# Performance work log

Hardware: AMD Instinct MI355X
Metric: run time of the kernel (lower is better)

## Reference

```python
import jax, jax.numpy as jnp
import numpy as np

N, F, H, F_ = 8192, 256, 2, 64
NEG_MASK = -1e10
LEAKY_SLOPE = 0.2


def setup_inputs() -> dict:
    key = jax.random.key(0)
    k0, k1, k2, k3 = jax.random.split(key, 4)
    X = jax.random.normal(k0, (N, F), jnp.float32)
    A = (jax.random.uniform(k1, (N, N)) < 0.01).astype(jnp.float32)
    A = jnp.maximum(A, jnp.eye(N, dtype=jnp.float32))
    W = jax.random.normal(k2, (H, F, F_), jnp.float32) * (1.0 / np.sqrt(F))
    b = jnp.zeros((H, F_), jnp.float32)
    a = jax.random.normal(k3, (H, F_), jnp.float32) * 0.1
    return {"X": X, "A": A, "W": W, "b": b, "a": a}


def reference(X, A, W, b, a):
    # per-head projected features: [H, N, F_]
    feats = jnp.einsum('nf,hfo->hno', X, W)
    # score[h,i,j] = sum_o feats[h,i,o] * feats[h,j,o] * a[h,o]
    # (identical math to Dot(axes=-1)([X_0*X_1, a^T]) without the [N,N,F_] tensor)
    scores = jnp.einsum('hno,hmo->hnm', feats * a[:, None, :], feats)
    scores = jax.nn.leaky_relu(scores, negative_slope=LEAKY_SLOPE)
    scores = scores + NEG_MASK * (1.0 - A)  # adjacency mask (broadcast over heads)
    attn = jax.nn.softmax(scores, axis=-1)  # [H, N, N]
    # dropout_rate=0 -> identity at inference
    out = jnp.einsum('hnm,hmo->hno', attn, feats) + b[:, None, :]  # [H, N, F_]
    out = jnp.transpose(out, (1, 0, 2)).reshape(X.shape[0], H * F_)  # concat heads
    return jax.nn.relu(out)
```

## Files before the change

kernel.cpp:

```cpp
#include <hip/hip_runtime.h>

#define NN 8192
#define FIN 256
#define FO 64
#define CAP 192

typedef float nf4 __attribute__((ext_vector_type(4)));

__global__ __launch_bounds__(256) void feats_kernel(
    const float* __restrict__ X,
    const float* __restrict__ W,
    float* __restrict__ feats)
{
    __shared__ float Ws[128*FO];
    __shared__ float Xs[32*132];
    const int h = blockIdx.y;
    const int row0 = blockIdx.x * 32;
    const int t = threadIdx.x;
    const int rg = t >> 4;
    const int c0 = (t & 15) << 2;
    float acc0[4] = {0.f,0.f,0.f,0.f};
    float acc1[4] = {0.f,0.f,0.f,0.f};

    for (int kp = 0; kp < 2; ++kp){
        const int kb = kp * 128;
        const float* Wh = W + h*FIN*FO + kb*FO;
        #pragma unroll
        for (int it=0; it<8; ++it){
            int flat = (it*256 + t)*4;
            *(float4*)&Ws[flat] = *(const float4*)&Wh[flat];
        }
        #pragma unroll
        for (int it=0; it<4; ++it){
            int flat = (it*256 + t)*4;
            int r = flat >> 7, f0 = flat & 127;
            *(float4*)&Xs[r*132 + f0] = *(const float4*)&X[(size_t)(row0+r)*FIN + kb + f0];
        }
        __syncthreads();
        const float* xp0 = &Xs[(rg*2+0)*132];
        const float* xp1 = &Xs[(rg*2+1)*132];
        #pragma unroll 4
        for (int k=0; k<128; ++k){
            float x0 = xp0[k], x1 = xp1[k];
            float4 w4 = *(const float4*)&Ws[k*FO + c0];
            acc0[0]=fmaf(x0,w4.x,acc0[0]); acc0[1]=fmaf(x0,w4.y,acc0[1]);
            acc0[2]=fmaf(x0,w4.z,acc0[2]); acc0[3]=fmaf(x0,w4.w,acc0[3]);
            acc1[0]=fmaf(x1,w4.x,acc1[0]); acc1[1]=fmaf(x1,w4.y,acc1[1]);
            acc1[2]=fmaf(x1,w4.z,acc1[2]); acc1[3]=fmaf(x1,w4.w,acc1[3]);
        }
        __syncthreads();
    }
    float* o0 = feats + ((size_t)(row0 + rg*2 + 0)*2 + h)*FO + c0;
    float* o1 = feats + ((size_t)(row0 + rg*2 + 1)*2 + h)*FO + c0;
    *(float4*)o0 = make_float4(acc0[0],acc0[1],acc0[2],acc0[3]);
    *(float4*)o1 = make_float4(acc1[0],acc1[1],acc1[2],acc1[3]);
}

__global__ __launch_bounds__(256) void gat_kernel(
    const float* __restrict__ A,
    const float* __restrict__ feats,
    const float* __restrict__ av,
    const float* __restrict__ bv,
    float* __restrict__ out)
{
    __shared__ int   nsh[4][CAP];
    __shared__ float sc[4][2][CAP];

    const int w   = threadIdx.x >> 6;
    const int l   = threadIdx.x & 63;
    const int i   = (blockIdx.x << 2) + w;
    const int gi  = l >> 5;
    const int l32 = l & 31;

    int*   ns = nsh[w];
    float* s0 = sc[w][0];
    float* s1 = sc[w][1];

    float4 qa = *(const float4*)&av[l32*4];
    float4 qf = *(const float4*)&feats[(size_t)i*128 + l32*4];
    const float4 q4 = make_float4(qf.x*qa.x, qf.y*qa.y, qf.z*qa.z, qf.w*qa.w);

    const nf4* Arow4 = (const nf4*)(A + (size_t)i*NN);
    const unsigned long long ltmask = (1ull << l) - 1ull;
    int base = 0;
    #pragma unroll 1
    for (int round = 0; round < 4; ++round){
        nf4 v[8];
        #pragma unroll
        for (int r=0; r<8; ++r)
            v[r] = __builtin_nontemporal_load(&Arow4[(round*8+r)*64 + l]);
        #pragma unroll
        for (int r=0; r<8; ++r){
            unsigned long long m0 = __ballot(v[r].x != 0.0f);
            unsigned long long m1 = __ballot(v[r].y != 0.0f);
            unsigned long long m2 = __ballot(v[r].z != 0.0f);
            unsigned long long m3 = __ballot(v[r].w != 0.0f);
            int p0 = __popcll(m0), p1 = __popcll(m1), p2 = __popcll(m2), p3 = __popcll(m3);
            const int colb = ((round*8+r)*64 + l)*4;
            if ((m0>>l)&1){ int p = base + __popcll(m0 & ltmask); if (p<CAP) ns[p] = colb;   } base += p0;
            if ((m1>>l)&1){ int p = base + __popcll(m1 & ltmask); if (p<CAP) ns[p] = colb+1; } base += p1;
            if ((m2>>l)&1){ int p = base + __popcll(m2 & ltmask); if (p<CAP) ns[p] = colb+2; } base += p2;
            if ((m3>>l)&1){ int p = base + __popcll(m3 & ltmask); if (p<CAP) ns[p] = colb+3; } base += p3;
        }
    }
    const int n = min(base, CAP);

    for (int k0 = gi*4; k0 < n; k0 += 8){
        const int kn = min(4, n - k0);
        float4 f[4];
        #pragma unroll
        for (int u=0; u<4; ++u){
            int j = (u < kn) ? ns[k0+u] : i;
            f[u] = *(const float4*)&feats[(size_t)j*128 + l32*4];
        }
        #pragma unroll
        for (int u=0; u<4; ++u){
            float d = f[u].x*q4.x + f[u].y*q4.y + f[u].z*q4.z + f[u].w*q4.w;
            d += __shfl_xor(d, 1, 64);
            d += __shfl_xor(d, 2, 64);
            d += __shfl_xor(d, 4, 64);
            d += __shfl_xor(d, 8, 64);
            d = (d >= 0.f) ? d : 0.2f*d;
            if (u < kn){
                if (l32 == 0)  s0[k0+u] = d;
                if (l32 == 16) s1[k0+u] = d;
            }
        }
    }

    float* ss = (l < 32) ? s0 : s1;
    float mx = -1e30f;
    for (int k = l32; k < n; k += 32) mx = fmaxf(mx, ss[k]);
    #pragma unroll
    for (int off = 16; off; off >>= 1) mx = fmaxf(mx, __shfl_xor(mx, off, 64));
    float sum = 0.f;
    for (int k = l32; k < n; k += 32){ float p = __expf(ss[k] - mx); ss[k] = p; sum += p; }
    #pragma unroll
    for (int off = 16; off; off >>= 1) sum += __shfl_xor(sum, off, 64);

    const int o2 = l * 2;
    const float* ps = ss;
    float2 acc = make_float2(0.f, 0.f);
    int k = 0;
    for (; k + 4 <= n; k += 4){
        int j0 = ns[k], j1 = ns[k+1], j2 = ns[k+2], j3 = ns[k+3];
        float2 f0 = *(const float2*)&feats[(size_t)j0*128 + o2];
        float2 f1 = *(const float2*)&feats[(size_t)j1*128 + o2];
        float2 f2 = *(const float2*)&feats[(size_t)j2*128 + o2];
        float2 f3 = *(const float2*)&feats[(size_t)j3*128 + o2];
        float p0 = ps[k], p1 = ps[k+1], p2 = ps[k+2], p3 = ps[k+3];
        acc.x = fmaf(p0, f0.x, acc.x); acc.y = fmaf(p0, f0.y, acc.y);
        acc.x = fmaf(p1, f1.x, acc.x); acc.y = fmaf(p1, f1.y, acc.y);
        acc.x = fmaf(p2, f2.x, acc.x); acc.y = fmaf(p2, f2.y, acc.y);
        acc.x = fmaf(p3, f3.x, acc.x); acc.y = fmaf(p3, f3.y, acc.y);
    }
    for (; k < n; ++k){
        int j = ns[k];
        float2 f = *(const float2*)&feats[(size_t)j*128 + o2];
        float p = ps[k];
        acc.x = fmaf(p, f.x, acc.x); acc.y = fmaf(p, f.y, acc.y);
    }

    float2 bb = *(const float2*)&bv[o2];
    float inv = 1.0f / sum;
    float2 r;
    r.x = fmaxf(fmaf(acc.x, inv, bb.x), 0.f);
    r.y = fmaxf(fmaf(acc.y, inv, bb.y), 0.f);
    *(float2*)&out[(size_t)i*128 + o2] = r;
}

extern "C" void kernel_launch(void* const* d_in, const int* in_sizes, int n_in,
                              void* d_out, int out_size, void* d_ws, size_t ws_size,
                              hipStream_t stream) {
    const float* X = (const float*)d_in[0];
    const float* A = (const float*)d_in[1];
    const float* W = (const float*)d_in[2];
    const float* b = (const float*)d_in[3];
    const float* a = (const float*)d_in[4];
    float* out = (float*)d_out;

    float* feats = (float*)d_ws;

    feats_kernel<<<dim3(NN/32, 2), 256, 0, stream>>>(X, W, feats);
    gat_kernel  <<<dim3(NN/4),     256, 0, stream>>>(A, feats, a, b, out);
}
```

Baseline: 392.2 us.

## Fuse score, softmax and aggregation into single-pass online softmax

```diff
diff --git a/kernel.cpp b/kernel.cpp
--- a/kernel.cpp
+++ b/kernel.cpp
@@ -63,40 +63,36 @@
     const float* __restrict__ bv,
     float* __restrict__ out)
 {
-    __shared__ int   nsh[4][CAP];
-    __shared__ float sc[4][2][CAP];
+    __shared__ int nsh[4][CAP];
 
-    const int w   = threadIdx.x >> 6;
-    const int l   = threadIdx.x & 63;
-    const int i   = (blockIdx.x << 2) + w;
-    const int gi  = l >> 5;
-    const int l32 = l & 31;
+    const int w  = threadIdx.x >> 6;
+    const int l  = threadIdx.x & 63;
+    const int i  = (blockIdx.x << 2) + w;
+    const int o2 = l << 1;
 
-    int*   ns = nsh[w];
-    float* s0 = sc[w][0];
-    float* s1 = sc[w][1];
+    int* ns = nsh[w];
 
-    float4 qa = *(const float4*)&av[l32*4];
-    float4 qf = *(const float4*)&feats[(size_t)i*128 + l32*4];
-    const float4 q4 = make_float4(qf.x*qa.x, qf.y*qa.y, qf.z*qa.z, qf.w*qa.w);
+    float2 qa = *(const float2*)&av[o2];
+    float2 qf = *(const float2*)&feats[(size_t)i*128 + o2];
+    const float2 q2 = make_float2(qf.x*qa.x, qf.y*qa.y);
 
     const nf4* Arow4 = (const nf4*)(A + (size_t)i*NN);
     const unsigned long long ltmask = (1ull << l) - 1ull;
     int base = 0;
     #pragma unroll 1
-    for (int round = 0; round < 4; ++round){
-        nf4 v[8];
+    for (int round = 0; round < 8; ++round){
+        nf4 v[4];
         #pragma unroll
-        for (int r=0; r<8; ++r)
-            v[r] = __builtin_nontemporal_load(&Arow4[(round*8+r)*64 + l]);
+        for (int r=0; r<4; ++r)
+            v[r] = __builtin_nontemporal_load(&Arow4[(round*4+r)*64 + l]);
         #pragma unroll
-        for (int r=0; r<8; ++r){
+        for (int r=0; r<4; ++r){
             unsigned long long m0 = __ballot(v[r].x != 0.0f);
             unsigned long long m1 = __ballot(v[r].y != 0.0f);
             unsigned long long m2 = __ballot(v[r].z != 0.0f);
             unsigned long long m3 = __ballot(v[r].w != 0.0f);
             int p0 = __popcll(m0), p1 = __popcll(m1), p2 = __popcll(m2), p3 = __popcll(m3);
-            const int colb = ((round*8+r)*64 + l)*4;
+            const int colb = ((round*4+r)*64 + l)*4;
             if ((m0>>l)&1){ int p = base + __popcll(m0 & ltmask); if (p<CAP) ns[p] = colb;   } base += p0;
             if ((m1>>l)&1){ int p = base + __popcll(m1 & ltmask); if (p<CAP) ns[p] = colb+1; } base += p1;
             if ((m2>>l)&1){ int p = base + __popcll(m2 & ltmask); if (p<CAP) ns[p] = colb+2; } base += p2;
@@ -105,64 +101,43 @@
     }
     const int n = min(base, CAP);
 
-    for (int k0 = gi*4; k0 < n; k0 += 8){
-        const int kn = min(4, n - k0);
-        float4 f[4];
+    float m = -1e30f, s = 0.f;
+    float2 acc = make_float2(0.f, 0.f);
+
+    for (int k = 0; k < n; k += 4){
+        float2 f[4]; float d[4];
         #pragma unroll
         for (int u=0; u<4; ++u){
-            int j = (u < kn) ? ns[k0+u] : i;
-            f[u] = *(const float4*)&feats[(size_t)j*128 + l32*4];
+            int j = (k+u < n) ? ns[k+u] : i;
+            f[u] = *(const float2*)&feats[(size_t)j*128 + o2];
         }
         #pragma unroll
         for (int u=0; u<4; ++u){
-            float d = f[u].x*q4.x + f[u].y*q4.y + f[u].z*q4.z + f[u].w*q4.w;
-            d += __shfl_xor(d, 1, 64);
-            d += __shfl_xor(d, 2, 64);
-            d += __shfl_xor(d, 4, 64);
-            d += __shfl_xor(d, 8, 64);
-            d = (d >= 0.f) ? d : 0.2f*d;
-            if (u < kn){
-                if (l32 == 0)  s0[k0+u] = d;
-                if (l32 == 16) s1[k0+u] = d;
-            }
+            float dd = f[u].x*q2.x + f[u].y*q2.y;
+            dd += __shfl_xor(dd, 1, 64);
+            dd += __shfl_xor(dd, 2, 64);
+            dd += __shfl_xor(dd, 4, 64);
+            dd += __shfl_xor(dd, 8, 64);
+            dd += __shfl_xor(dd, 16, 64);
+            dd = (dd >= 0.f) ? dd : 0.2f*dd;
+            d[u] = (k+u < n) ? dd : -1e30f;
+        }
+        float dm = fmaxf(fmaxf(d[0], d[1]), fmaxf(d[2], d[3]));
+        if (dm > m){
+            float r = __expf(m - dm);
+            acc.x *= r; acc.y *= r; s *= r; m = dm;
+        }
+        #pragma unroll
+        for (int u=0; u<4; ++u){
+            float p = __expf(d[u] - m);
+            s += p;
+            acc.x = fmaf(p, f[u].x, acc.x);
+            acc.y = fmaf(p, f[u].y, acc.y);
         }
     }
 
-    float* ss = (l < 32) ? s0 : s1;
-    float mx = -1e30f;
-    for (int k = l32; k < n; k += 32) mx = fmaxf(mx, ss[k]);
-    #pragma unroll
-    for (int off = 16; off; off >>= 1) mx = fmaxf(mx, __shfl_xor(mx, off, 64));
-    float sum = 0.f;
-    for (int k = l32; k < n; k += 32){ float p = __expf(ss[k] - mx); ss[k] = p; sum += p; }
-    #pragma unroll
-    for (int off = 16; off; off >>= 1) sum += __shfl_xor(sum, off, 64);
-
-    const int o2 = l * 2;
-    const float* ps = ss;
-    float2 acc = make_float2(0.f, 0.f);
-    int k = 0;
-    for (; k + 4 <= n; k += 4){
-        int j0 = ns[k], j1 = ns[k+1], j2 = ns[k+2], j3 = ns[k+3];
-        float2 f0 = *(const float2*)&feats[(size_t)j0*128 + o2];
-        float2 f1 = *(const float2*)&feats[(size_t)j1*128 + o2];
-        float2 f2 = *(const float2*)&feats[(size_t)j2*128 + o2];
-        float2 f3 = *(const float2*)&feats[(size_t)j3*128 + o2];
-        float p0 = ps[k], p1 = ps[k+1], p2 = ps[k+2], p3 = ps[k+3];
-        acc.x = fmaf(p0, f0.x, acc.x); acc.y = fmaf(p0, f0.y, acc.y);
-        acc.x = fmaf(p1, f1.x, acc.x); acc.y = fmaf(p1, f1.y, acc.y);
-        acc.x = fmaf(p2, f2.x, acc.x); acc.y = fmaf(p2, f2.y, acc.y);
-        acc.x = fmaf(p3, f3.x, acc.x); acc.y = fmaf(p3, f3.y, acc.y);
-    }
-    for (; k < n; ++k){
-        int j = ns[k];
-        float2 f = *(const float2*)&feats[(size_t)j*128 + o2];
-        float p = ps[k];
-        acc.x = fmaf(p, f.x, acc.x); acc.y = fmaf(p, f.y, acc.y);
-    }
-
     float2 bb = *(const float2*)&bv[o2];
-    float inv = 1.0f / sum;
+    float inv = 1.0f / s;
     float2 r;
     r.x = fmaxf(fmaf(acc.x, inv, bb.x), 0.f);
     r.y = fmaxf(fmaf(acc.y, inv, bb.y), 0.f);
```

Result: no change. 394.9 us (+0.7%).
